# Optimization experiments

Measured on AMD Instinct MI355X. Metric: run time of the kernel, lower is better.

## Reference

```python
import jax, jax.numpy as jnp
import numpy as np

BETA, HIDDEN, C_DIM = 512, 512, 256
HP, WP, B = 64, 64, 64


def setup_inputs() -> dict:
    key = jax.random.key(0)
    ks = jax.random.split(key, 8)
    s = 0.02
    return {
        "V": jax.random.normal(ks[0], (HP, WP, C_DIM, B), dtype=jnp.float32),
        "h_t": jax.random.normal(ks[1], (B, 1, HIDDEN), dtype=jnp.float32),
        "W_h_w": jax.random.normal(ks[2], (BETA, HIDDEN), dtype=jnp.float32) * s,
        "W_h_b": jax.random.normal(ks[3], (BETA,), dtype=jnp.float32) * s,
        "W_w": jax.random.normal(ks[4], (BETA, C_DIM), dtype=jnp.float32) * s,
        "W_b": jax.random.normal(ks[5], (BETA,), dtype=jnp.float32) * s,
        "beta_w": jax.random.normal(ks[6], (1, BETA), dtype=jnp.float32) * s,
        "beta_b": jax.random.normal(ks[7], (1,), dtype=jnp.float32) * s,
    }


def reference(V, h_t, W_h_w, W_h_b, W_w, W_b, beta_w, beta_b):
    Hp, Wp, C, batch = V.shape
    # [B, HW, C]
    V_new = jnp.transpose(V, (3, 0, 1, 2)).reshape(batch, Hp * Wp, C)
    # U_T = W_h(h_t) + W(V_new): [B,1,beta] + [B,HW,beta]
    U_T = (h_t @ W_h_w.T + W_h_b) + (V_new @ W_w.T + W_b)
    # E_t: [B, HW, 1]
    E_t = jnp.tanh(U_T) @ beta_w.T + beta_b
    # softmax over the HW positions (dim=1), then transpose -> [B, 1, HW]
    A_t = jax.nn.softmax(E_t, axis=1)
    # weighted sum: [B, 1, C]
    C_T = jnp.einsum('bsk,bsc->bkc', A_t, V_new)
    return C_T
```

## Files before the change

### kernel.cpp

```cpp
#include <hip/hip_runtime.h>

typedef float f32x4 __attribute__((ext_vector_type(4)));
typedef short s16x8 __attribute__((ext_vector_type(8)));
typedef unsigned int u32;
typedef u32 u32x4 __attribute__((ext_vector_type(4)));
typedef unsigned long long u64;
typedef unsigned short ush;

#define CD    256
#define NB    64
#define NBETA 512
#define NHID  512
#define PPB   32

__device__ __forceinline__ ush f2bf(float x) {
    u32 u = __builtin_bit_cast(u32, x);
    u += 0x7fffu + ((u >> 16) & 1u);
    return (ush)(u >> 16);
}
__device__ __forceinline__ float bf2f(ush h) {
    u32 u = ((u32)h) << 16;
    return __builtin_bit_cast(float, u);
}
__device__ __forceinline__ u32 cvtpk(float lo, float hi) {
    u32 r;
    asm("v_cvt_pk_bf16_f32 %0, %1, %2" : "=v"(r) : "v"(lo), "v"(hi));
    return r;
}
__device__ __forceinline__ float fexp2(float x) {
    float r;
    asm("v_exp_f32 %0, %1" : "=v"(r) : "v"(x));
    return r;
}

__global__ __launch_bounds__(512) void prep_kernel(
    const float* __restrict__ h_t, const float* __restrict__ W_h_w,
    const float* __restrict__ W_h_b, const float* __restrict__ W_w,
    const float* __restrict__ W_b,
    ush* __restrict__ hws, ush* __restrict__ wwb)
{
    const int blk = blockIdx.x;
    const int tid = threadIdx.x;
    if (blk < NB) {
        __shared__ float hrow[NHID];
        hrow[tid] = h_t[blk * NHID + tid];
        __syncthreads();
        const float* wr = W_h_w + tid * NHID;
        float a0 = 0.f, a1 = 0.f, a2 = 0.f, a3 = 0.f;
        #pragma unroll 4
        for (int h = 0; h < NHID; h += 4) {
            f32x4 wv = *(const f32x4*)(wr + h);
            a0 = fmaf(wv.x, hrow[h], a0);
            a1 = fmaf(wv.y, hrow[h + 1], a1);
            a2 = fmaf(wv.z, hrow[h + 2], a2);
            a3 = fmaf(wv.w, hrow[h + 3], a3);
        }
        float acc = (a0 + a1) + (a2 + a3) + W_h_b[tid] + W_b[tid];
        hws[blk * NBETA + tid] = f2bf(acc);
    } else {
        const int idx = ((blk - NB) * 512 + tid) * 8;
        f32x4 a = *(const f32x4*)(W_w + idx);
        f32x4 b = *(const f32x4*)(W_w + idx + 4);
        s16x8 pk;
        pk[0] = (short)f2bf(a.x); pk[1] = (short)f2bf(a.y);
        pk[2] = (short)f2bf(a.z); pk[3] = (short)f2bf(a.w);
        pk[4] = (short)f2bf(b.x); pk[5] = (short)f2bf(b.y);
        pk[6] = (short)f2bf(b.z); pk[7] = (short)f2bf(b.w);
        *(s16x8*)(wwb + idx) = pk;
    }
}

__global__ __launch_bounds__(512, 2) void fused(
    const float* __restrict__ V,
    const ush* __restrict__ wwb,
    const ush* __restrict__ hws,
    const float* __restrict__ beta_w,
    const float* __restrict__ beta_b,
    float* __restrict__ num,
    float* __restrict__ lsum)
{
    __shared__ __align__(16) char VtB[3][16384];
    __shared__ float nbS[NBETA];
    __shared__ __align__(16) float ewP[2][8][2][16][4];

    const int tid = threadIdx.x;
    const int l = tid & 63, w = tid >> 6, g = l >> 4, r = l & 15;
    const int bl = tid & 31, cs = tid >> 5;
    const int bh = blockIdx.x & 1, chunk = blockIdx.x >> 1;

    nbS[tid] = -2.f * beta_w[tid];
    const float bbias = beta_b[0];

    float base = 0.f;
    #pragma unroll
    for (int m = 0; m < 4; ++m) {
        f32x4 t = *(const f32x4*)(beta_w + w * 64 + m * 16 + g * 4);
        base += (t.x + t.y) + (t.z + t.w);
    }

    const ush* wbase = wwb + (size_t)(w * 64 + r) * CD + g * 8;
    s16x8 a[4][8];
    #pragma unroll
    for (int m = 0; m < 4; ++m)
        #pragma unroll
        for (int ks = 0; ks < 8; ++ks)
            a[m][ks] = *(const s16x8*)(wbase + m * (16 * CD) + ks * 32);

    const ush* hbase = hws + (size_t)(bh * 32 + r) * NBETA + w * 64 + g * 4;
    u64 ua[4][2];
    #pragma unroll
    for (int m = 0; m < 4; ++m)
        #pragma unroll
        for (int n = 0; n < 2; ++n)
            ua[m][n] = *(const u64*)(hbase + n * (16 * NBETA) + m * 16);

    const int p0 = chunk * PPB;
    const float* vbase = V + (size_t)p0 * (CD * NB) + bh * 32 + bl;
    const int wswz = (bl & 15) << 4;
    const int rswz = r << 4;

    float cacc[16];
    #pragma unroll
    for (int j = 0; j < 16; ++j) cacc[j] = 0.f;
    float lacc = 0.f;

    float nv[16];

    {
        #pragma unroll
        for (int j = 0; j < 16; ++j)
            nv[j] = __builtin_nontemporal_load(vbase + (cs * 16 + j) * NB);
        char* db = VtB[0] + bl * 512;
        u32x4 pk0 = {cvtpk(nv[0], nv[1]), cvtpk(nv[2], nv[3]),
                     cvtpk(nv[4], nv[5]), cvtpk(nv[6], nv[7])};
        *(u32x4*)(db + ((cs * 32) ^ wswz)) = pk0;
        u32x4 pk1 = {cvtpk(nv[8], nv[9]), cvtpk(nv[10], nv[11]),
                     cvtpk(nv[12], nv[13]), cvtpk(nv[14], nv[15])};
        *(u32x4*)(db + ((cs * 32 + 16) ^ wswz)) = pk1;
    }
    {
        const float* vp = vbase + (size_t)(CD * NB);
        #pragma unroll
        for (int j = 0; j < 16; ++j)
            nv[j] = __builtin_nontemporal_load(vp + (cs * 16 + j) * NB);
    }
    __syncthreads();

    int cur = 0, nxt = 16384;
    for (int i = 0; i < PPB; ++i) {
        const char* vt = VtB[0] + cur;

        if (i + 1 < PPB) {
            char* db = VtB[0] + nxt + bl * 512;
            u32x4 pk0 = {cvtpk(nv[0], nv[1]), cvtpk(nv[2], nv[3]),
                         cvtpk(nv[4], nv[5]), cvtpk(nv[6], nv[7])};
            *(u32x4*)(db + ((cs * 32) ^ wswz)) = pk0;
            u32x4 pk1 = {cvtpk(nv[8], nv[9]), cvtpk(nv[10], nv[11]),
                         cvtpk(nv[12], nv[13]), cvtpk(nv[14], nv[15])};
            *(u32x4*)(db + ((cs * 32 + 16) ^ wswz)) = pk1;
        }
        if (i + 2 < PPB) {
            const float* vp = vbase + (size_t)(i + 2) * (CD * NB);
            #pragma unroll
            for (int j = 0; j < 16; ++j)
                nv[j] = __builtin_nontemporal_load(vp + (cs * 16 + j) * NB);
        }

        const char* vrow = vt + r * 512;

        f32x4 acc0[4];
        #pragma unroll
        for (int m = 0; m < 4; ++m) {
            u64 h = ua[m][0];
            acc0[m] = (f32x4){bf2f((ush)h), bf2f((ush)(h >> 16)),
                              bf2f((ush)(h >> 32)), bf2f((ush)(h >> 48))};
        }
        __builtin_amdgcn_s_setprio(1);
        #pragma unroll
        for (int ks = 0; ks < 8; ++ks) {
            const int off = ((ks << 6) | (g << 4)) ^ rswz;
            s16x8 b0 = *(const s16x8*)(vrow + off);
            #pragma unroll
            for (int m = 0; m < 4; ++m)
                acc0[m] = __builtin_amdgcn_mfma_f32_16x16x32_bf16(a[m][ks], b0, acc0[m], 0, 0, 0);
        }
        __builtin_amdgcn_s_setprio(0);
        float pe0 = base;
        #pragma unroll
        for (int m = 0; m < 4; ++m) {
            f32x4 nbv = *(const f32x4*)(&nbS[w * 64 + m * 16 + g * 4]);
            #pragma unroll
            for (int q = 0; q < 4; ++q) {
                float s = __builtin_amdgcn_rcpf(
                    1.f + fexp2(acc0[m][q] * 2.8853900817779268f));
                pe0 = fmaf(nbv[q], s, pe0);
            }
        }

        f32x4 acc1[4];
        #pragma unroll
        for (int m = 0; m < 4; ++m) {
            u64 h = ua[m][1];
            acc1[m] = (f32x4){bf2f((ush)h), bf2f((ush)(h >> 16)),
                              bf2f((ush)(h >> 32)), bf2f((ush)(h >> 48))};
        }
        __builtin_amdgcn_s_setprio(1);
        #pragma unroll
        for (int ks = 0; ks < 8; ++ks) {
            const int off = ((ks << 6) | (g << 4)) ^ rswz;
            s16x8 b1 = *(const s16x8*)(vrow + 8192 + off);
            #pragma unroll
            for (int m = 0; m < 4; ++m)
                acc1[m] = __builtin_amdgcn_mfma_f32_16x16x32_bf16(a[m][ks], b1, acc1[m], 0, 0, 0);
        }
        __builtin_amdgcn_s_setprio(0);
        float pe1 = base;
        #pragma unroll
        for (int m = 0; m < 4; ++m) {
            f32x4 nbv = *(const f32x4*)(&nbS[w * 64 + m * 16 + g * 4]);
            #pragma unroll
            for (int q = 0; q < 4; ++q) {
                float s = __builtin_amdgcn_rcpf(
                    1.f + fexp2(acc1[m][q] * 2.8853900817779268f));
                pe1 = fmaf(nbv[q], s, pe1);
            }
        }

        ewP[i & 1][w][0][r][g] = pe0;
        ewP[i & 1][w][1][r][g] = pe1;

        __syncthreads();

        {
            const int n_ = bl >> 4, r_ = bl & 15;
            float e = bbias;
            #pragma unroll
            for (int wv = 0; wv < 8; ++wv) {
                f32x4 t = *(const f32x4*)(&ewP[i & 1][wv][n_][r_][0]);
                e += (t.x + t.y) + (t.z + t.w);
            }
            float wgt = __expf(e);
            lacc += wgt;
            const char* vb = vt + bl * 512;
            #pragma unroll
            for (int k = 0; k < 2; ++k) {
                s16x8 v = *(const s16x8*)(vb + ((cs * 32 + k * 16) ^ wswz));
                #pragma unroll
                for (int j = 0; j < 8; ++j)
                    cacc[k * 8 + j] = fmaf(wgt, bf2f((ush)v[j]), cacc[k * 8 + j]);
            }
        }

        cur = nxt;
        nxt += 16384;
        if (nxt == 49152) nxt = 0;
    }

    float* np = num + (size_t)blockIdx.x * (32 * CD) + bl * CD + cs * 16;
    #pragma unroll
    for (int k = 0; k < 4; ++k)
        *(f32x4*)(np + k * 4) =
            (f32x4){cacc[k * 4], cacc[k * 4 + 1], cacc[k * 4 + 2], cacc[k * 4 + 3]};
    if (cs == 0) lsum[blockIdx.x * 32 + bl] = lacc;
}

__global__ __launch_bounds__(256) void combine4(
    const float* __restrict__ num, const float* __restrict__ lsum,
    float* __restrict__ out)
{
    __shared__ float rs[4][64];
    __shared__ float rl[4][64];
    const int b = blockIdx.x >> 2, cq = blockIdx.x & 3;
    const int bh = b >> 5, blr = b & 31;
    const int cl = threadIdx.x & 63, kq = threadIdx.x >> 6;

    float s = 0.f, ls = 0.f;
    #pragma unroll 4
    for (int ch = kq * 32; ch < kq * 32 + 32; ++ch) {
        const int blk = ch * 2 + bh;
        s += num[(size_t)blk * (32 * CD) + blr * CD + cq * 64 + cl];
        ls += lsum[blk * 32 + blr];
    }
    rs[kq][cl] = s; rl[kq][cl] = ls;
    __syncthreads();
    if (kq == 0) {
        float sn = rs[0][cl] + rs[1][cl] + rs[2][cl] + rs[3][cl];
        float sl = rl[0][cl] + rl[1][cl] + rl[2][cl] + rl[3][cl];
        out[b * CD + cq * 64 + cl] = sn / sl;
    }
}

extern "C" void kernel_launch(void* const* d_in, const int* in_sizes, int n_in,
                              void* d_out, int out_size, void* d_ws, size_t ws_size,
                              hipStream_t stream)
{
    (void)in_sizes; (void)n_in; (void)out_size; (void)ws_size;
    const float* V      = (const float*)d_in[0];
    const float* h_t    = (const float*)d_in[1];
    const float* W_h_w  = (const float*)d_in[2];
    const float* W_h_b  = (const float*)d_in[3];
    const float* W_w    = (const float*)d_in[4];
    const float* W_b    = (const float*)d_in[5];
    const float* beta_w = (const float*)d_in[6];
    const float* beta_b = (const float*)d_in[7];

    char* ws = (char*)d_ws;
    ush*   wwb = (ush*)ws;
    ush*   hws = (ush*)(ws + 262144);
    float* num = (float*)(ws + 262144 + 65536);
    float* lsm = (float*)(ws + 262144 + 65536 + 8388608);

    hipLaunchKernelGGL(prep_kernel, dim3(96), dim3(512), 0, stream,
                       h_t, W_h_w, W_h_b, W_w, W_b, hws, wwb);
    hipLaunchKernelGGL(fused, dim3(256), dim3(512), 0, stream,
                       V, wwb, hws, beta_w, beta_b, num, lsm);
    hipLaunchKernelGGL(combine4, dim3(256), dim3(256), 0, stream,
                       num, lsm, (float*)d_out);
}
```

Baseline: 139.1 us.

## Defer softmax-weighted accumulation by one iteration to overlap with MFMA

Moves the per-position weight reduction and the weighted V accumulation from after the barrier into the start of the next iteration, operating on the previous slot of the triple-buffered LDS tile, so it can interleave with the next MFMA block instead of sitting on the critical path after the sync. It also splits the tanh/score dot-product into two independent accumulators to shorten the dependency chain, and stores each partial score right after it is computed. The reordering relies on the three-slot LDS ring and the double-buffered ewP keeping the previous data alive for one more iteration. It adds a tail epilogue and raises register pressure slightly.

```diff
diff --git a/kernel.cpp b/kernel.cpp
--- a/kernel.cpp
+++ b/kernel.cpp
@@ -126,6 +126,27 @@
 
     float nv[16];
 
+#define WSUM(PAR, SLOT)                                                       \
+    {                                                                         \
+        const int n_ = bl >> 4, r_ = bl & 15;                                 \
+        float e = bbias;                                                      \
+        _Pragma("unroll")                                                     \
+        for (int wv = 0; wv < 8; ++wv) {                                      \
+            f32x4 t = *(const f32x4*)(&ewP[PAR][wv][n_][r_][0]);              \
+            e += (t.x + t.y) + (t.z + t.w);                                   \
+        }                                                                     \
+        float wgt = __expf(e);                                                \
+        lacc += wgt;                                                          \
+        const char* vb = VtB[0] + (SLOT) + bl * 512;                          \
+        _Pragma("unroll")                                                     \
+        for (int k = 0; k < 2; ++k) {                                         \
+            s16x8 v = *(const s16x8*)(vb + ((cs * 32 + k * 16) ^ wswz));      \
+            _Pragma("unroll")                                                 \
+            for (int j = 0; j < 8; ++j)                                       \
+                cacc[k * 8 + j] = fmaf(wgt, bf2f((ush)v[j]), cacc[k * 8 + j]);\
+        }                                                                     \
+    }
+
     {
         #pragma unroll
         for (int j = 0; j < 16; ++j)
@@ -146,6 +167,7 @@
     }
     __syncthreads();
 
+    int prv = 32768;
     int cur = 0, nxt = 16384;
     for (int i = 0; i < PPB; ++i) {
         const char* vt = VtB[0] + cur;
@@ -166,6 +188,8 @@
                 nv[j] = __builtin_nontemporal_load(vp + (cs * 16 + j) * NB);
         }
 
+        if (i > 0) WSUM((i - 1) & 1, prv)
+
         const char* vrow = vt + r * 512;
 
         f32x4 acc0[4];
@@ -185,16 +209,20 @@
                 acc0[m] = __builtin_amdgcn_mfma_f32_16x16x32_bf16(a[m][ks], b0, acc0[m], 0, 0, 0);
         }
         __builtin_amdgcn_s_setprio(0);
-        float pe0 = base;
-        #pragma unroll
-        for (int m = 0; m < 4; ++m) {
-            f32x4 nbv = *(const f32x4*)(&nbS[w * 64 + m * 16 + g * 4]);
-            #pragma unroll
-            for (int q = 0; q < 4; ++q) {
-                float s = __builtin_amdgcn_rcpf(
-                    1.f + fexp2(acc0[m][q] * 2.8853900817779268f));
-                pe0 = fmaf(nbv[q], s, pe0);
+        {
+            float peA = 0.f, peB = 0.f;
+            #pragma unroll
+            for (int m = 0; m < 4; ++m) {
+                f32x4 nbv = *(const f32x4*)(&nbS[w * 64 + m * 16 + g * 4]);
+                #pragma unroll
+                for (int q = 0; q < 4; ++q) {
+                    float s = __builtin_amdgcn_rcpf(
+                        1.f + fexp2(acc0[m][q] * 2.8853900817779268f));
+                    if (m < 2) peA = fmaf(nbv[q], s, peA);
+                    else       peB = fmaf(nbv[q], s, peB);
+                }
             }
+            ewP[i & 1][w][0][r][g] = base + peA + peB;
         }
 
         f32x4 acc1[4];
@@ -214,47 +242,33 @@
                 acc1[m] = __builtin_amdgcn_mfma_f32_16x16x32_bf16(a[m][ks], b1, acc1[m], 0, 0, 0);
         }
         __builtin_amdgcn_s_setprio(0);
-        float pe1 = base;
-        #pragma unroll
-        for (int m = 0; m < 4; ++m) {
-            f32x4 nbv = *(const f32x4*)(&nbS[w * 64 + m * 16 + g * 4]);
-            #pragma unroll
-            for (int q = 0; q < 4; ++q) {
-                float s = __builtin_amdgcn_rcpf(
-                    1.f + fexp2(acc1[m][q] * 2.8853900817779268f));
-                pe1 = fmaf(nbv[q], s, pe1);
+        {
+            float peA = 0.f, peB = 0.f;
+            #pragma unroll
+            for (int m = 0; m < 4; ++m) {
+                f32x4 nbv = *(const f32x4*)(&nbS[w * 64 + m * 16 + g * 4]);
+                #pragma unroll
+                for (int q = 0; q < 4; ++q) {
+                    float s = __builtin_amdgcn_rcpf(
+                        1.f + fexp2(acc1[m][q] * 2.8853900817779268f));
+                    if (m < 2) peA = fmaf(nbv[q], s, peA);
+                    else       peB = fmaf(nbv[q], s, peB);
+                }
             }
-        }
-
-        ewP[i & 1][w][0][r][g] = pe0;
-        ewP[i & 1][w][1][r][g] = pe1;
+            ewP[i & 1][w][1][r][g] = base + peA + peB;
+        }
 
         __syncthreads();
 
-        {
-            const int n_ = bl >> 4, r_ = bl & 15;
-            float e = bbias;
-            #pragma unroll
-            for (int wv = 0; wv < 8; ++wv) {
-                f32x4 t = *(const f32x4*)(&ewP[i & 1][wv][n_][r_][0]);
-                e += (t.x + t.y) + (t.z + t.w);
-            }
-            float wgt = __expf(e);
-            lacc += wgt;
-            const char* vb = vt + bl * 512;
-            #pragma unroll
-            for (int k = 0; k < 2; ++k) {
-                s16x8 v = *(const s16x8*)(vb + ((cs * 32 + k * 16) ^ wswz));
-                #pragma unroll
-                for (int j = 0; j < 8; ++j)
-                    cacc[k * 8 + j] = fmaf(wgt, bf2f((ush)v[j]), cacc[k * 8 + j]);
-            }
-        }
-
+        prv = cur;
         cur = nxt;
         nxt += 16384;
         if (nxt == 49152) nxt = 0;
     }
+
+    WSUM((PPB - 1) & 1, prv)
+
+#undef WSUM
 
     float* np = num + (size_t)blockIdx.x * (32 * CD) + bl * CD + cs * 16;
     #pragma unroll
```

New measurement: 140.3 us. No clear change (+0.9%).
